# Kernel tuning notes

Hardware: AMD Instinct MI355X
Metric: run time of the kernel (lower is better)

## Reference

```python
import jax, jax.numpy as jnp
import numpy as np

N_HEADS = 16


def _rope(x, cos, sin):
    # x: (B,H,S,hd); cos,sin: (1,1,S,hd//2). Full-dim rotation (rot_dim == head_dim).
    xe = x[..., 0::2]
    xo = x[..., 1::2]
    re = xe * cos - xo * sin
    ro = xe * sin + xo * cos
    return jnp.stack([re, ro], axis=-1).reshape(x.shape)


def setup_inputs() -> dict:
    key = jax.random.key(0)
    B, S, D = 2, 2048, 1024
    hd = D // N_HEADS
    k1, k2, k3, k4, k5 = jax.random.split(key, 5)
    x = jax.random.normal(k1, (B, S, D), dtype=jnp.float32)
    # Linear params (lecun-normal-ish scale)
    w_qkv = jax.random.normal(k2, (D, 3 * D), dtype=jnp.float32) / np.sqrt(D)
    b_qkv = jnp.zeros((3 * D,), dtype=jnp.float32)
    w_out = jax.random.normal(k3, (D, D), dtype=jnp.float32) / np.sqrt(D)
    b_out = jnp.zeros((D,), dtype=jnp.float32)
    # Rotary tables: (S, hd//2)
    inv_freq = 1.0 / (10000.0 ** (np.arange(0, hd, 2, dtype=np.float32) / hd))
    angles = jnp.asarray(np.arange(S, dtype=np.float32)[:, None] * inv_freq[None, :])
    cos = jnp.cos(angles)
    sin = jnp.sin(angles)
    # Causal mask (seq, seq), True = attend
    mask = jnp.tril(jnp.ones((S, S), dtype=bool))
    return {"x": x, "w_qkv": w_qkv, "b_qkv": b_qkv, "w_out": w_out,
            "b_out": b_out, "cos": cos, "sin": sin, "mask": mask}


def reference(x, w_qkv, b_qkv, w_out, b_out, cos, sin, mask):
    B, S, D = x.shape
    H = N_HEADS
    hd = D // H
    scale = hd ** (-0.5)
    qkv = x @ w_qkv + b_qkv  # (B,S,3D)
    qkv = qkv.reshape(B, S, 3, H, hd).transpose(2, 0, 3, 1, 4)  # (3,B,H,S,hd)
    q, k, v = qkv[0], qkv[1], qkv[2]
    c = cos[None, None, :, :]
    s = sin[None, None, :, :]
    q = _rope(q, c, s)
    k = _rope(k, c, s)
    attn = jnp.einsum('bhqd,bhkd->bhqk', q, k) * scale
    attn = jnp.where(mask, attn, -1e9)
    attn = jax.nn.softmax(attn, axis=-1)
    out = jnp.einsum('bhqk,bhkd->bhqd', attn, v)
    out = out.transpose(0, 2, 1, 3).reshape(B, S, D)
    return out @ w_out + b_out
```

## Files before the change

### kernel.cpp

```cpp
#include <hip/hip_runtime.h>
#include <stdint.h>

typedef unsigned short u16;
typedef __attribute__((ext_vector_type(8))) __bf16 bf16x8;
typedef __attribute__((ext_vector_type(4))) float f32x4;
typedef __attribute__((ext_vector_type(4))) unsigned short u16x4;

__device__ __forceinline__ float bf2f(u16 u){
  unsigned int x = ((unsigned int)u) << 16;
  return __builtin_bit_cast(float, x);
}
__device__ __forceinline__ u16 f2bf(float f){
  return __builtin_bit_cast(u16, (__bf16)f);
}
__device__ __forceinline__ float fexp2(float x){ return __builtin_exp2f(x); }
__device__ __forceinline__ void lds_load16(const void* g, void* l){
  __builtin_amdgcn_global_load_lds(
      (const __attribute__((address_space(1))) unsigned int*)g,
      (__attribute__((address_space(3))) unsigned int*)l, 16, 0, 0);
}

__device__ __forceinline__ void transpose_body(const float* __restrict__ in,
                                               u16* __restrict__ out,
                                               int R, int C, int bx, int by,
                                               u16 (*t)[65]){
  const int c0 = bx * 64, r0 = by * 64;
  const int tid = threadIdx.x;
  const int rr = tid >> 3;
  const int cc = (tid & 7) * 8;
#pragma unroll
  for (int i = 0; i < 2; i++){
    int r = i * 32 + rr;
    const float* p = in + (size_t)(r0 + r) * C + c0 + cc;
    f32x4 v0 = *(const f32x4*)p;
    f32x4 v1 = *(const f32x4*)(p + 4);
#pragma unroll
    for (int j = 0; j < 4; j++){ t[r][cc + j] = f2bf(v0[j]); t[r][cc + 4 + j] = f2bf(v1[j]); }
  }
  __syncthreads();
#pragma unroll
  for (int i = 0; i < 2; i++){
    int c = i * 32 + rr;
    u16 tmp[8];
#pragma unroll
    for (int j = 0; j < 8; j++) tmp[j] = t[cc + j][c];
    *(bf16x8*)(out + (size_t)(c0 + c) * R + r0 + cc) = *(const bf16x8*)tmp;
  }
}

__global__ __launch_bounds__(256) void prep(const float* __restrict__ w_qkv,
                                            const float* __restrict__ w_out,
                                            const float* __restrict__ x,
                                            u16* __restrict__ wT1,
                                            u16* __restrict__ wT2,
                                            u16* __restrict__ xbf){
  __shared__ u16 t[64][65];
  const int bid = blockIdx.x;
  if (bid < 2048){
    int i = bid * 256 + threadIdx.x;
    const float* p = x + (size_t)i * 8;
    f32x4 v0 = *(const f32x4*)p;
    f32x4 v1 = *(const f32x4*)(p + 4);
    u16 tmp[8];
#pragma unroll
    for (int j = 0; j < 4; j++){ tmp[j] = f2bf(v0[j]); tmp[4 + j] = f2bf(v1[j]); }
    *(bf16x8*)(xbf + (size_t)i * 8) = *(const bf16x8*)tmp;
  } else if (bid < 2048 + 768){
    int idx = bid - 2048;
    transpose_body(w_qkv, wT1, 1024, 3072, idx % 48, idx / 48, t);
  } else {
    int idx = bid - 2816;
    transpose_body(w_out, wT2, 1024, 1024, idx % 16, idx / 16, t);
  }
}

__global__ __launch_bounds__(256) void v_transpose(const u16* __restrict__ qkv,
                                                   u16* __restrict__ vT){
  const int S = 2048, LD = 3072;
  __shared__ u16 t[64][65];
  const int bh = blockIdx.y;
  const int b = bh >> 4, h = bh & 15;
  const int s0 = blockIdx.x * 64;
  const u16* src = qkv + (size_t)b * S * LD + 2048 + h * 64;
  const int tid = threadIdx.x;
  const int rr = tid >> 3;
  const int cc = (tid & 7) * 8;
#pragma unroll
  for (int i = 0; i < 2; i++){
    int s = i * 32 + rr;
    bf16x8 v = *(const bf16x8*)(src + (size_t)(s0 + s) * LD + cc);
#pragma unroll
    for (int j = 0; j < 8; j++) t[s][cc + j] = __builtin_bit_cast(u16, (__bf16)v[j]);
  }
  __syncthreads();
  u16* dst = vT + (size_t)bh * 64 * S;
#pragma unroll
  for (int i = 0; i < 2; i++){
    int d = i * 32 + rr;
    u16 tmp[8];
#pragma unroll
    for (int j = 0; j < 8; j++) tmp[j] = t[cc + j][d];
    *(bf16x8*)(dst + (size_t)d * S + s0 + cc) = *(const bf16x8*)tmp;
  }
}

template<bool OUTF32, bool ROPE>
__global__ __launch_bounds__(256, 3) void gemm_bt(const u16* __restrict__ A,
                                                  const u16* __restrict__ Bt,
                                                  const float* __restrict__ bias,
                                                  void* __restrict__ Cv,
                                                  int M, int N, int K,
                                                  const float* __restrict__ cosb,
                                                  const float* __restrict__ sinb){
  __shared__ u16 As[128 * 32];
  __shared__ u16 Bs[128 * 32];
  const int nx = gridDim.x;
  const int L = blockIdx.x + nx * blockIdx.y;
  const int per = (nx * gridDim.y) >> 3;
  const int wg = (L & 7) * per + (L >> 3);
  const int bn = wg % nx, bm = wg / nx;
  const int tid = threadIdx.x, w = tid >> 6, l = tid & 63;
  const int lo = l & 15, hi = l >> 4;
  const int wr = (w >> 1) * 64, wc = (w & 1) * 64;
  f32x4 acc[4][4] = {};
  const int lrow = l >> 2, lcd = l & 3;

  for (int k0 = 0; k0 < K; k0 += 32){
#pragma unroll
    for (int i = 0; i < 2; i++){
      int row0 = i * 64 + w * 16;
      int row = row0 + lrow;
      int cs = lcd ^ ((row >> 1) & 3);
      lds_load16(A  + (size_t)(bm * 128 + row) * K + k0 + cs * 8,
                 (char*)As + row0 * 64);
      lds_load16(Bt + (size_t)(bn * 128 + row) * K + k0 + cs * 8,
                 (char*)Bs + row0 * 64);
    }
    __syncthreads();
    bf16x8 a[4], b[4];
#pragma unroll
    for (int mi = 0; mi < 4; mi++){
      int row = wr + mi * 16 + lo;
      unsigned byte = (unsigned)(row * 64 + hi * 16) ^ (((row >> 1) & 3) << 4);
      a[mi] = *(const bf16x8*)((const char*)As + byte);
    }
#pragma unroll
    for (int ni = 0; ni < 4; ni++){
      int row = wc + ni * 16 + lo;
      unsigned byte = (unsigned)(row * 64 + hi * 16) ^ (((row >> 1) & 3) << 4);
      b[ni] = *(const bf16x8*)((const char*)Bs + byte);
    }
    __builtin_amdgcn_s_setprio(1);
#pragma unroll
    for (int mi = 0; mi < 4; mi++)
#pragma unroll
      for (int ni = 0; ni < 4; ni++)
        acc[mi][ni] = __builtin_amdgcn_mfma_f32_16x16x32_bf16(a[mi], b[ni], acc[mi][ni], 0, 0, 0);
    __builtin_amdgcn_s_setprio(0);
    __syncthreads();
  }
  if (ROPE && bn < 16){
#pragma unroll
    for (int mi = 0; mi < 4; mi++){
#pragma unroll
      for (int r = 0; r < 4; r++){
        int grow = bm * 128 + wr + mi * 16 + hi * 4 + r;
        int stok = grow & 2047;
#pragma unroll
        for (int ni = 0; ni < 4; ni++){
          int col = bn * 128 + wc + ni * 16 + lo;
          float v = acc[mi][ni][r] + bias[col];
          float partner = __shfl_xor(v, 1, 64);
          int ip = (col & 63) >> 1;
          float c = cosb[stok * 32 + ip], sn = sinb[stok * 32 + ip];
          float res = (lo & 1) ? (partner * sn + v * c) : (v * c - partner * sn);
          ((u16*)Cv)[(size_t)grow * N + col] = f2bf(res);
        }
      }
    }
  } else {
#pragma unroll
    for (int mi = 0; mi < 4; mi++){
#pragma unroll
      for (int r = 0; r < 4; r++){
        int grow = bm * 128 + wr + mi * 16 + hi * 4 + r;
#pragma unroll
        for (int ni = 0; ni < 4; ni++){
          int col = bn * 128 + wc + ni * 16 + lo;
          float v = acc[mi][ni][r] + bias[col];
          if (OUTF32)
            ((float*)Cv)[(size_t)grow * N + col] = v;
          else
            ((u16*)Cv)[(size_t)grow * N + col] = f2bf(v);
        }
      }
    }
  }
}

#define FA_PHASE(T_, OA_, OB_, MA_, MB_, LA_, LB_)                             \
  {                                                                            \
    const int q0p = (T_) * 32;                                                 \
    const int qrA = q0p + lo, qrB = q0p + 16 + lo;                             \
    const int nkt = (T_) + 1;                                                  \
    const int ch = (nkt + 1) >> 1;                                             \
    const int k0 = w ? ch : 0;                                                 \
    const int k1 = w ? nkt : ch;                                               \
    bf16x8 qfA0, qfA1, qfB0, qfB1;                                             \
    {                                                                          \
      bf16x8 va0 = *(const bf16x8*)(Qp + (size_t)qrA * LD + hi * 8);           \
      bf16x8 va1 = *(const bf16x8*)(Qp + (size_t)qrA * LD + 32 + hi * 8);      \
      bf16x8 vb0 = *(const bf16x8*)(Qp + (size_t)qrB * LD + hi * 8);           \
      bf16x8 vb1 = *(const bf16x8*)(Qp + (size_t)qrB * LD + 32 + hi * 8);      \
      _Pragma("unroll")                                                        \
      for (int j = 0; j < 8; j++){                                             \
        qfA0[j] = (__bf16)((float)va0[j] * QSC);                               \
        qfA1[j] = (__bf16)((float)va1[j] * QSC);                               \
        qfB0[j] = (__bf16)((float)vb0[j] * QSC);                               \
        qfB1[j] = (__bf16)((float)vb1[j] * QSC);                               \
      }                                                                        \
    }                                                                          \
    float lparA = 0.f, lparB = 0.f;                                            \
    MA_ = -1e30f; MB_ = -1e30f;                                                \
    if (k0 < k1){                                                              \
      _Pragma("unroll")                                                        \
      for (int i = 0; i < 4; i++)                                              \
        lds_load16(Kp + (size_t)(k0 * 32 + i * 8 + srow8) * LD + scs * 8,      \
                   (char*)&Ks[w][0][0] + i * 1024);                            \
    }                                                                          \
    int cur = 0;                                                               \
    for (int kt = k0; kt < k1; kt++){                                          \
      bf16x8 vb[4];                                                            \
      _Pragma("unroll")                                                        \
      for (int fd = 0; fd < 4; fd++)                                           \
        vb[fd] = *(const bf16x8*)(Vb + (size_t)(fd * 16 + lo) * S +            \
                                  kt * 32 + hi * 8);                           \
      bf16x8 kb[2][2];                                                         \
      _Pragma("unroll")                                                        \
      for (int c = 0; c < 2; c++){                                             \
        _Pragma("unroll")                                                      \
        for (int f = 0; f < 2; f++){                                           \
          int srw = f * 16 + lo;                                               \
          unsigned byte = ((unsigned)(srw * 128 + c * 64 + hi * 16)) ^         \
                          ((lo & 7) << 4);                                     \
          kb[c][f] = *(const bf16x8*)((const char*)&Ks[w][cur][0] + byte);     \
        }                                                                      \
      }                                                                        \
      if (kt + 1 < k1){                                                        \
        _Pragma("unroll")                                                      \
        for (int i = 0; i < 4; i++)                                            \
          lds_load16(Kp + (size_t)((kt + 1) * 32 + i * 8 + srow8) * LD +       \
                         scs * 8,                                              \
                     (char*)&Ks[w][cur ^ 1][0] + i * 1024);                    \
      }                                                                        \
      f32x4 saA[2] = {}, saB[2] = {};                                          \
      __builtin_amdgcn_s_setprio(1);                                           \
      _Pragma("unroll")                                                        \
      for (int f = 0; f < 2; f++){                                             \
        saA[f] = __builtin_amdgcn_mfma_f32_16x16x32_bf16(kb[0][f], qfA0,       \
                                                         saA[f], 0, 0, 0);     \
        saB[f] = __builtin_amdgcn_mfma_f32_16x16x32_bf16(kb[0][f], qfB0,       \
                                                         saB[f], 0, 0, 0);     \
        saA[f] = __builtin_amdgcn_mfma_f32_16x16x32_bf16(kb[1][f], qfA1,       \
                                                         saA[f], 0, 0, 0);     \
        saB[f] = __builtin_amdgcn_mfma_f32_16x16x32_bf16(kb[1][f], qfB1,       \
                                                         saB[f], 0, 0, 0);     \
      }                                                                        \
      __builtin_amdgcn_s_setprio(0);                                           \
      if (kt == nkt - 1){                                                      \
        _Pragma("unroll")                                                      \
        for (int f = 0; f < 2; f++){                                           \
          int key0 = kt * 32 + f * 16 + hi * 4;                                \
          _Pragma("unroll")                                                    \
          for (int r = 0; r < 4; r++){                                         \
            if (key0 + r > qrA) saA[f][r] = -1e30f;                            \
            if (key0 + r > qrB) saB[f][r] = -1e30f;                            \
          }                                                                    \
        }                                                                      \
      }                                                                        \
      float pmA = fmaxf(                                                       \
          fmaxf(fmaxf(saA[0][0], saA[0][1]), fmaxf(saA[0][2], saA[0][3])),     \
          fmaxf(fmaxf(saA[1][0], saA[1][1]), fmaxf(saA[1][2], saA[1][3])));    \
      float pmB = fmaxf(                                                       \
          fmaxf(fmaxf(saB[0][0], saB[0][1]), fmaxf(saB[0][2], saB[0][3])),     \
          fmaxf(fmaxf(saB[1][0], saB[1][1]), fmaxf(saB[1][2], saB[1][3])));    \
      if (!__all(fmaxf(pmA - MA_, pmB - MB_) <= 11.5f)){                       \
        float rmA = fmaxf(pmA, __shfl_xor(pmA, 16, 64));                       \
        rmA = fmaxf(rmA, __shfl_xor(rmA, 32, 64));                             \
        float rmB = fmaxf(pmB, __shfl_xor(pmB, 16, 64));                       \
        rmB = fmaxf(rmB, __shfl_xor(rmB, 32, 64));                             \
        float mnA = fmaxf(MA_, rmA), mnB = fmaxf(MB_, rmB);                    \
        float cA = fexp2(MA_ - mnA), cB = fexp2(MB_ - mnB);                    \
        MA_ = mnA; MB_ = mnB;                                                  \
        lparA *= cA; lparB *= cB;                                              \
        float cqA[4], cqB[4];                                                  \
        _Pragma("unroll")                                                      \
        for (int r = 0; r < 4; r++){                                           \
          cqA[r] = __shfl(cA, hi * 4 + r, 64);                                 \
          cqB[r] = __shfl(cB, hi * 4 + r, 64);                                 \
        }                                                                      \
        _Pragma("unroll")                                                      \
        for (int fd = 0; fd < 4; fd++){                                        \
          _Pragma("unroll")                                                    \
          for (int r = 0; r < 4; r++){                                         \
            OA_[fd][r] *= cqA[r]; OB_[fd][r] *= cqB[r];                        \
          }                                                                    \
        }                                                                      \
      }                                                                        \
      float pvA[2][4], pvB[2][4];                                              \
      _Pragma("unroll")                                                        \
      for (int f = 0; f < 2; f++){                                             \
        _Pragma("unroll")                                                      \
        for (int r = 0; r < 4; r++){                                           \
          pvA[f][r] = fexp2(saA[f][r] - MA_);                                  \
          pvB[f][r] = fexp2(saB[f][r] - MB_);                                  \
        }                                                                      \
      }                                                                        \
      _Pragma("unroll")                                                        \
      for (int f = 0; f < 2; f++){                                             \
        u16x4 pkA, pkB;                                                        \
        _Pragma("unroll")                                                      \
        for (int r = 0; r < 4; r++){                                           \
          pkA[r] = f2bf(pvA[f][r]); pkB[r] = f2bf(pvB[f][r]);                  \
        }                                                                      \
        *(u16x4*)((char*)&Ps[w][0][0] + lo * 72 + f * 32 + hi * 8) = pkA;      \
        *(u16x4*)((char*)&Ps[w][1][0] + lo * 72 + f * 32 + hi * 8) = pkB;      \
      }                                                                        \
      lparA += ((pvA[0][0] + pvA[0][1]) + (pvA[0][2] + pvA[0][3]))             \
             + ((pvA[1][0] + pvA[1][1]) + (pvA[1][2] + pvA[1][3]));            \
      lparB += ((pvB[0][0] + pvB[0][1]) + (pvB[0][2] + pvB[0][3]))             \
             + ((pvB[1][0] + pvB[1][1]) + (pvB[1][2] + pvB[1][3]));            \
      bf16x8 paA = *(const bf16x8*)((const char*)&Ps[w][0][0] + lo * 72 +      \
                                    hi * 16);                                  \
      bf16x8 paB = *(const bf16x8*)((const char*)&Ps[w][1][0] + lo * 72 +      \
                                    hi * 16);                                  \
      __builtin_amdgcn_s_setprio(1);                                           \
      _Pragma("unroll")                                                        \
      for (int fd = 0; fd < 4; fd++){                                          \
        OA_[fd] = __builtin_amdgcn_mfma_f32_16x16x32_bf16(paA, vb[fd],         \
                                                          OA_[fd], 0, 0, 0);   \
        OB_[fd] = __builtin_amdgcn_mfma_f32_16x16x32_bf16(paB, vb[fd],         \
                                                          OB_[fd], 0, 0, 0);   \
      }                                                                        \
      __builtin_amdgcn_s_setprio(0);                                           \
      cur ^= 1;                                                                \
    }                                                                          \
    lparA += __shfl_xor(lparA, 16, 64); lparA += __shfl_xor(lparA, 32, 64);    \
    lparB += __shfl_xor(lparB, 16, 64); lparB += __shfl_xor(lparB, 32, 64);    \
    LA_ = lparA; LB_ = lparB;                                                  \
  }

#define FA_WRITEPART(slot_, OA_, OB_, MA_, MB_, LA_, LB_)                      \
  {                                                                            \
    _Pragma("unroll")                                                          \
    for (int fd = 0; fd < 4; fd++){                                            \
      u16x4 pkA, pkB;                                                          \
      _Pragma("unroll")                                                        \
      for (int r = 0; r < 4; r++){                                             \
        pkA[r] = f2bf(OA_[fd][r]); pkB[r] = f2bf(OB_[fd][r]);                  \
      }                                                                        \
      *(u16x4*)((char*)&Xo[slot_][0] + (fd * 16 + lo) * 72 + hi * 8) = pkA;    \
      *(u16x4*)((char*)&Xo[slot_][0] + (fd * 16 + lo) * 72 + 32 + hi * 8) = pkB;\
    }                                                                          \
    if (hi == 0){                                                              \
      Xm[slot_][lo] = MA_;      Xl[slot_][lo] = LA_;                           \
      Xm[slot_][16 + lo] = MB_; Xl[slot_][16 + lo] = LB_;                      \
    }                                                                          \
  }

#define FA_COMBINE(slot_, T_, OA_, OB_, MA_, MB_, LA_, LB_)                    \
  {                                                                            \
    const int q0p = (T_) * 32;                                                 \
    u16x4 pA[4], pB[4];                                                        \
    _Pragma("unroll")                                                          \
    for (int fd = 0; fd < 4; fd++){                                            \
      pA[fd] = *(const u16x4*)((const char*)&Xo[slot_][0] +                    \
                               (fd * 16 + lo) * 72 + hi * 8);                  \
      pB[fd] = *(const u16x4*)((const char*)&Xo[slot_][0] +                    \
                               (fd * 16 + lo) * 72 + 32 + hi * 8);             \
    }                                                                          \
    _Pragma("unroll")                                                          \
    for (int r = 0; r < 4; r++){                                               \
      float mOA = __shfl(MA_, hi * 4 + r, 64);                                 \
      float lOA = __shfl(LA_, hi * 4 + r, 64);                                 \
      float mOB = __shfl(MB_, hi * 4 + r, 64);                                 \
      float lOB = __shfl(LB_, hi * 4 + r, 64);                                 \
      float mPA = Xm[slot_][hi * 4 + r], lPA = Xl[slot_][hi * 4 + r];          \
      float mPB = Xm[slot_][16 + hi * 4 + r], lPB = Xl[slot_][16 + hi * 4 + r];\
      float MfA = fmaxf(mOA, mPA), MfB = fmaxf(mOB, mPB);                      \
      float c0A = fexp2(mOA - MfA), c1A = fexp2(mPA - MfA);                    \
      float c0B = fexp2(mOB - MfB), c1B = fexp2(mPB - MfB);                    \
      float invA = 1.0f / (lOA * c0A + lPA * c1A);                             \
      float invB = 1.0f / (lOB * c0B + lPB * c1B);                             \
      int srA = q0p + hi * 4 + r;                                              \
      int srB = q0p + 16 + hi * 4 + r;                                         \
      u16* orA = Oout + (size_t)(b * S + srA) * 1024 + h * 64;                 \
      u16* orB = Oout + (size_t)(b * S + srB) * 1024 + h * 64;                 \
      _Pragma("unroll")                                                        \
      for (int fd = 0; fd < 4; fd++){                                          \
        float vA = (OA_[fd][r] * c0A + bf2f(pA[fd][r]) * c1A) * invA;          \
        float vB = (OB_[fd][r] * c0B + bf2f(pB[fd][r]) * c1B) * invB;          \
        orA[fd * 16 + lo] = f2bf(vA);                                          \
        orB[fd * 16 + lo] = f2bf(vB);                                          \
      }                                                                        \
    }                                                                          \
  }

__global__ __launch_bounds__(128, 2) void flash_attn(const u16* __restrict__ qkv,
                                                     const u16* __restrict__ vT,
                                                     u16* __restrict__ Oout){
  const int S = 2048, LD = 3072;
  const int L = blockIdx.x;
  const int bh = L & 31;
  const int bx = L >> 5;
  const int b = bh >> 4, h = bh & 15;
  const u16* base = qkv + (size_t)b * S * LD;
  const u16* Qp = base + h * 64;
  const u16* Kp = base + 1024 + h * 64;
  const u16* Vb = vT + (size_t)bh * 64 * S;
  const int tid = threadIdx.x, w = tid >> 6, l = tid & 63;
  const int lo = l & 15, hi = l >> 4;
  __shared__ u16 Ks[2][2][32 * 64];
  __shared__ u16 Ps[2][2][16 * 36];
  __shared__ u16 Xo[2][64 * 36];
  __shared__ float Xm[2][32], Xl[2][32];

  const float QSC = 0.125f * 1.44269504089f;
  const int srow8 = l >> 3;
  const int scs = (l & 7) ^ srow8;

  f32x4 o1A[4] = {}, o1B[4] = {};
  f32x4 o2A[4] = {}, o2B[4] = {};
  float m1A, m1B, l1A, l1B, m2A, m2B, l2A, l2B;

  FA_PHASE(63 - bx, o1A, o1B, m1A, m1B, l1A, l1B);
  if (w == 1) FA_WRITEPART(0, o1A, o1B, m1A, m1B, l1A, l1B);
  FA_PHASE(bx,      o2A, o2B, m2A, m2B, l2A, l2B);
  if (w == 0) FA_WRITEPART(1, o2A, o2B, m2A, m2B, l2A, l2B);
  __syncthreads();
  if (w == 0){
    FA_COMBINE(0, 63 - bx, o1A, o1B, m1A, m1B, l1A, l1B);
  } else {
    FA_COMBINE(1, bx,      o2A, o2B, m2A, m2B, l2A, l2B);
  }
}

extern "C" void kernel_launch(void* const* d_in, const int* in_sizes, int n_in,
                              void* d_out, int out_size, void* d_ws, size_t ws_size,
                              hipStream_t stream){
  const float* x     = (const float*)d_in[0];
  const float* w_qkv = (const float*)d_in[1];
  const float* b_qkv = (const float*)d_in[2];
  const float* w_out = (const float*)d_in[3];
  const float* b_out = (const float*)d_in[4];
  const float* cosb  = (const float*)d_in[5];
  const float* sinb  = (const float*)d_in[6];
  float* out = (float*)d_out;
  char* ws = (char*)d_ws;
  u16* qkv  = (u16*)(ws);
  u16* attn = (u16*)(ws + 25165824);
  u16* xbf  = attn;
  u16* wT2  = (u16*)(ws + 33554432);
  u16* wT1  = (u16*)(ws + 35651584);
  u16* vT   = (u16*)(ws + 35651584);

  prep<<<3072, 256, 0, stream>>>(w_qkv, w_out, x, wT1, wT2, xbf);
  gemm_bt<false, true ><<<dim3(24, 32), 256, 0, stream>>>(xbf, wT1, b_qkv, qkv,
                                                          4096, 3072, 1024, cosb, sinb);
  v_transpose<<<dim3(32, 32), 256, 0, stream>>>(qkv, vT);
  flash_attn<<<1024, 128, 0, stream>>>(qkv, vT, attn);
  gemm_bt<true , false><<<dim3(8, 32), 256, 0, stream>>>(attn, wT2, b_out, out,
                                                         4096, 1024, 1024, cosb, sinb);
}
```

Measured before the change: 129.3 us.

## Deepen K prefetch pipeline with register double-buffered LDS reads in flash attention

Restructures the attention K loop into a manually unrolled two-iteration body. The next tile's K fragments are read from LDS into alternate register sets during the current QK MFMAs, and the global-to-LDS staging is issued two tiles ahead. This aims to hide LDS read latency and global load latency behind MFMA work. It adds register pressure and relies on the LDS double buffer being consistent, since no explicit waits are visible between staging and reading.

```diff
diff --git a/kernel.cpp b/kernel.cpp
--- a/kernel.cpp
+++ b/kernel.cpp
@@ -198,6 +198,123 @@
   }
 }
 
+#define FA_DSREAD(KB_, KT_)                                                    \
+  { _Pragma("unroll")                                                          \
+    for (int c = 0; c < 2; c++){                                               \
+      _Pragma("unroll")                                                        \
+      for (int f = 0; f < 2; f++){                                             \
+        int srw = f * 16 + lo;                                                 \
+        unsigned byte = ((unsigned)(srw * 128 + c * 64 + hi * 16)) ^           \
+                        ((lo & 7) << 4);                                       \
+        KB_[c * 2 + f] = *(const bf16x8*)(                                     \
+            (const char*)&Ks[w][(KT_) & 1][0] + byte);                         \
+      } } }
+
+#define FA_STAGE(KT_)                                                          \
+  { _Pragma("unroll")                                                          \
+    for (int i = 0; i < 4; i++)                                                \
+      lds_load16(Kp + (size_t)((KT_) * 32 + i * 8 + srow8) * LD + scs * 8,     \
+                 (char*)&Ks[w][(KT_) & 1][0] + i * 1024); }
+
+#define FA_BODY(KBU_, KBL_, KT_, OA_, OB_, MA_, MB_)                           \
+  {                                                                            \
+    bf16x8 vb[4];                                                              \
+    _Pragma("unroll")                                                          \
+    for (int fd = 0; fd < 4; fd++)                                             \
+      vb[fd] = *(const bf16x8*)(Vb + (size_t)(fd * 16 + lo) * S +              \
+                                (KT_) * 32 + hi * 8);                          \
+    if ((KT_) + 1 < k1) FA_DSREAD(KBL_, (KT_) + 1);                            \
+    f32x4 saA[2] = {}, saB[2] = {};                                            \
+    __builtin_amdgcn_s_setprio(1);                                             \
+    saA[0] = __builtin_amdgcn_mfma_f32_16x16x32_bf16(KBU_[0], qfA0, saA[0], 0, 0, 0); \
+    saB[0] = __builtin_amdgcn_mfma_f32_16x16x32_bf16(KBU_[0], qfB0, saB[0], 0, 0, 0); \
+    saA[0] = __builtin_amdgcn_mfma_f32_16x16x32_bf16(KBU_[2], qfA1, saA[0], 0, 0, 0); \
+    saB[0] = __builtin_amdgcn_mfma_f32_16x16x32_bf16(KBU_[2], qfB1, saB[0], 0, 0, 0); \
+    saA[1] = __builtin_amdgcn_mfma_f32_16x16x32_bf16(KBU_[1], qfA0, saA[1], 0, 0, 0); \
+    saB[1] = __builtin_amdgcn_mfma_f32_16x16x32_bf16(KBU_[1], qfB0, saB[1], 0, 0, 0); \
+    saA[1] = __builtin_amdgcn_mfma_f32_16x16x32_bf16(KBU_[3], qfA1, saA[1], 0, 0, 0); \
+    saB[1] = __builtin_amdgcn_mfma_f32_16x16x32_bf16(KBU_[3], qfB1, saB[1], 0, 0, 0); \
+    __builtin_amdgcn_s_setprio(0);                                             \
+    __builtin_amdgcn_sched_barrier(0);                                         \
+    if ((KT_) + 2 < k1) FA_STAGE((KT_) + 2);                                   \
+    if ((KT_) == nkt - 1){                                                     \
+      _Pragma("unroll")                                                        \
+      for (int f = 0; f < 2; f++){                                             \
+        int key0 = (KT_) * 32 + f * 16 + hi * 4;                               \
+        _Pragma("unroll")                                                      \
+        for (int r = 0; r < 4; r++){                                           \
+          if (key0 + r > qrA) saA[f][r] = -1e30f;                              \
+          if (key0 + r > qrB) saB[f][r] = -1e30f;                              \
+        }                                                                      \
+      }                                                                        \
+    }                                                                          \
+    float pmA = fmaxf(                                                         \
+        fmaxf(fmaxf(saA[0][0], saA[0][1]), fmaxf(saA[0][2], saA[0][3])),       \
+        fmaxf(fmaxf(saA[1][0], saA[1][1]), fmaxf(saA[1][2], saA[1][3])));      \
+    float pmB = fmaxf(                                                         \
+        fmaxf(fmaxf(saB[0][0], saB[0][1]), fmaxf(saB[0][2], saB[0][3])),       \
+        fmaxf(fmaxf(saB[1][0], saB[1][1]), fmaxf(saB[1][2], saB[1][3])));      \
+    if (!__all(fmaxf(pmA - MA_, pmB - MB_) <= 11.5f)){                         \
+      float rmA = fmaxf(pmA, __shfl_xor(pmA, 16, 64));                         \
+      rmA = fmaxf(rmA, __shfl_xor(rmA, 32, 64));                               \
+      float rmB = fmaxf(pmB, __shfl_xor(pmB, 16, 64));                         \
+      rmB = fmaxf(rmB, __shfl_xor(rmB, 32, 64));                               \
+      float mnA = fmaxf(MA_, rmA), mnB = fmaxf(MB_, rmB);                      \
+      float cA = fexp2(MA_ - mnA), cB = fexp2(MB_ - mnB);                      \
+      MA_ = mnA; MB_ = mnB;                                                    \
+      lparA *= cA; lparB *= cB;                                                \
+      float cqA[4], cqB[4];                                                    \
+      _Pragma("unroll")                                                        \
+      for (int r = 0; r < 4; r++){                                             \
+        cqA[r] = __shfl(cA, hi * 4 + r, 64);                                   \
+        cqB[r] = __shfl(cB, hi * 4 + r, 64);                                   \
+      }                                                                        \
+      _Pragma("unroll")                                                        \
+      for (int fd = 0; fd < 4; fd++){                                          \
+        _Pragma("unroll")                                                      \
+        for (int r = 0; r < 4; r++){                                           \
+          OA_[fd][r] *= cqA[r]; OB_[fd][r] *= cqB[r];                          \
+        }                                                                      \
+      }                                                                        \
+    }                                                                          \
+    float pvA[2][4], pvB[2][4];                                                \
+    _Pragma("unroll")                                                          \
+    for (int f = 0; f < 2; f++){                                               \
+      _Pragma("unroll")                                                        \
+      for (int r = 0; r < 4; r++){                                             \
+        pvA[f][r] = fexp2(saA[f][r] - MA_);                                    \
+        pvB[f][r] = fexp2(saB[f][r] - MB_);                                    \
+      }                                                                        \
+    }                                                                          \
+    _Pragma("unroll")                                                          \
+    for (int f = 0; f < 2; f++){                                               \
+      u16x4 pkA, pkB;                                                          \
+      _Pragma("unroll")                                                        \
+      for (int r = 0; r < 4; r++){                                             \
+        pkA[r] = f2bf(pvA[f][r]); pkB[r] = f2bf(pvB[f][r]);                    \
+      }                                                                        \
+      *(u16x4*)((char*)&Ps[w][0][0] + lo * 72 + f * 32 + hi * 8) = pkA;        \
+      *(u16x4*)((char*)&Ps[w][1][0] + lo * 72 + f * 32 + hi * 8) = pkB;        \
+    }                                                                          \
+    lparA += ((pvA[0][0] + pvA[0][1]) + (pvA[0][2] + pvA[0][3]))               \
+           + ((pvA[1][0] + pvA[1][1]) + (pvA[1][2] + pvA[1][3]));              \
+    lparB += ((pvB[0][0] + pvB[0][1]) + (pvB[0][2] + pvB[0][3]))               \
+           + ((pvB[1][0] + pvB[1][1]) + (pvB[1][2] + pvB[1][3]));              \
+    bf16x8 paA = *(const bf16x8*)((const char*)&Ps[w][0][0] + lo * 72 +        \
+                                  hi * 16);                                    \
+    bf16x8 paB = *(const bf16x8*)((const char*)&Ps[w][1][0] + lo * 72 +        \
+                                  hi * 16);                                    \
+    __builtin_amdgcn_s_setprio(1);                                             \
+    _Pragma("unroll")                                                          \
+    for (int fd = 0; fd < 4; fd++){                                            \
+      OA_[fd] = __builtin_amdgcn_mfma_f32_16x16x32_bf16(paA, vb[fd],           \
+                                                        OA_[fd], 0, 0, 0);     \
+      OB_[fd] = __builtin_amdgcn_mfma_f32_16x16x32_bf16(paB, vb[fd],           \
+                                                        OB_[fd], 0, 0, 0);     \
+    }                                                                          \
+    __builtin_amdgcn_s_setprio(0);                                             \
+  }
+
 #define FA_PHASE(T_, OA_, OB_, MA_, MB_, LA_, LB_)                             \
   {                                                                            \
     const int q0p = (T_) * 32;                                                 \
@@ -222,128 +339,20 @@
     }                                                                          \
     float lparA = 0.f, lparB = 0.f;                                            \
     MA_ = -1e30f; MB_ = -1e30f;                                                \
-    if (k0 < k1){                                                              \
-      _Pragma("unroll")                                                        \
-      for (int i = 0; i < 4; i++)                                              \
-        lds_load16(Kp + (size_t)(k0 * 32 + i * 8 + srow8) * LD + scs * 8,      \
-                   (char*)&Ks[w][0][0] + i * 1024);                            \
-    }                                                                          \
-    int cur = 0;                                                               \
-    for (int kt = k0; kt < k1; kt++){                                          \
-      bf16x8 vb[4];                                                            \
-      _Pragma("unroll")                                                        \
-      for (int fd = 0; fd < 4; fd++)                                           \
-        vb[fd] = *(const bf16x8*)(Vb + (size_t)(fd * 16 + lo) * S +            \
-                                  kt * 32 + hi * 8);                           \
-      bf16x8 kb[2][2];                                                         \
-      _Pragma("unroll")                                                        \
-      for (int c = 0; c < 2; c++){                                             \
-        _Pragma("unroll")                                                      \
-        for (int f = 0; f < 2; f++){                                           \
-          int srw = f * 16 + lo;                                               \
-          unsigned byte = ((unsigned)(srw * 128 + c * 64 + hi * 16)) ^         \
-                          ((lo & 7) << 4);                                     \
-          kb[c][f] = *(const bf16x8*)((const char*)&Ks[w][cur][0] + byte);     \
-        }                                                                      \
-      }                                                                        \
-      if (kt + 1 < k1){                                                        \
-        _Pragma("unroll")                                                      \
-        for (int i = 0; i < 4; i++)                                            \
-          lds_load16(Kp + (size_t)((kt + 1) * 32 + i * 8 + srow8) * LD +       \
-                         scs * 8,                                              \
-                     (char*)&Ks[w][cur ^ 1][0] + i * 1024);                    \
-      }                                                                        \
-      f32x4 saA[2] = {}, saB[2] = {};                                          \
-      __builtin_amdgcn_s_setprio(1);                                           \
-      _Pragma("unroll")                                                        \
-      for (int f = 0; f < 2; f++){                                             \
-        saA[f] = __builtin_amdgcn_mfma_f32_16x16x32_bf16(kb[0][f], qfA0,       \
-                                                         saA[f], 0, 0, 0);     \
-        saB[f] = __builtin_amdgcn_mfma_f32_16x16x32_bf16(kb[0][f], qfB0,       \
-                                                         saB[f], 0, 0, 0);     \
-        saA[f] = __builtin_amdgcn_mfma_f32_16x16x32_bf16(kb[1][f], qfA1,       \
-                                                         saA[f], 0, 0, 0);     \
-        saB[f] = __builtin_amdgcn_mfma_f32_16x16x32_bf16(kb[1][f], qfB1,       \
-                                                         saB[f], 0, 0, 0);     \
-      }                                                                        \
-      __builtin_amdgcn_s_setprio(0);                                           \
-      if (kt == nkt - 1){                                                      \
-        _Pragma("unroll")                                                      \
-        for (int f = 0; f < 2; f++){                                           \
-          int key0 = kt * 32 + f * 16 + hi * 4;                                \
-          _Pragma("unroll")                                                    \
-          for (int r = 0; r < 4; r++){                                         \
-            if (key0 + r > qrA) saA[f][r] = -1e30f;                            \
-            if (key0 + r > qrB) saB[f][r] = -1e30f;                            \
-          }                                                                    \
-        }                                                                      \
-      }                                                                        \
-      float pmA = fmaxf(                                                       \
-          fmaxf(fmaxf(saA[0][0], saA[0][1]), fmaxf(saA[0][2], saA[0][3])),     \
-          fmaxf(fmaxf(saA[1][0], saA[1][1]), fmaxf(saA[1][2], saA[1][3])));    \
-      float pmB = fmaxf(                                                       \
-          fmaxf(fmaxf(saB[0][0], saB[0][1]), fmaxf(saB[0][2], saB[0][3])),     \
-          fmaxf(fmaxf(saB[1][0], saB[1][1]), fmaxf(saB[1][2], saB[1][3])));    \
-      if (!__all(fmaxf(pmA - MA_, pmB - MB_) <= 11.5f)){                       \
-        float rmA = fmaxf(pmA, __shfl_xor(pmA, 16, 64));                       \
-        rmA = fmaxf(rmA, __shfl_xor(rmA, 32, 64));                             \
-        float rmB = fmaxf(pmB, __shfl_xor(pmB, 16, 64));                       \
-        rmB = fmaxf(rmB, __shfl_xor(rmB, 32, 64));                             \
-        float mnA = fmaxf(MA_, rmA), mnB = fmaxf(MB_, rmB);                    \
-        float cA = fexp2(MA_ - mnA), cB = fexp2(MB_ - mnB);                    \
-        MA_ = mnA; MB_ = mnB;                                                  \
-        lparA *= cA; lparB *= cB;                                              \
-        float cqA[4], cqB[4];                                                  \
-        _Pragma("unroll")                                                      \
-        for (int r = 0; r < 4; r++){                                           \
-          cqA[r] = __shfl(cA, hi * 4 + r, 64);                                 \
-          cqB[r] = __shfl(cB, hi * 4 + r, 64);                                 \
-        }                                                                      \
-        _Pragma("unroll")                                                      \
-        for (int fd = 0; fd < 4; fd++){                                        \
-          _Pragma("unroll")                                                    \
-          for (int r = 0; r < 4; r++){                                         \
-            OA_[fd][r] *= cqA[r]; OB_[fd][r] *= cqB[r];                        \
-          }                                                                    \
-        }                                                                      \
-      }                                                                        \
-      float pvA[2][4], pvB[2][4];                                              \
-      _Pragma("unroll")                                                        \
-      for (int f = 0; f < 2; f++){                                             \
-        _Pragma("unroll")                                                      \
-        for (int r = 0; r < 4; r++){                                           \
-          pvA[f][r] = fexp2(saA[f][r] - MA_);                                  \
-          pvB[f][r] = fexp2(saB[f][r] - MB_);                                  \
-        }                                                                      \
-      }                                                                        \
-      _Pragma("unroll")                                                        \
-      for (int f = 0; f < 2; f++){                                             \
-        u16x4 pkA, pkB;                                                        \
-        _Pragma("unroll")                                                      \
-        for (int r = 0; r < 4; r++){                                           \
-          pkA[r] = f2bf(pvA[f][r]); pkB[r] = f2bf(pvB[f][r]);                  \
-        }                                                                      \
-        *(u16x4*)((char*)&Ps[w][0][0] + lo * 72 + f * 32 + hi * 8) = pkA;      \
-        *(u16x4*)((char*)&Ps[w][1][0] + lo * 72 + f * 32 + hi * 8) = pkB;      \
-      }                                                                        \
-      lparA += ((pvA[0][0] + pvA[0][1]) + (pvA[0][2] + pvA[0][3]))             \
-             + ((pvA[1][0] + pvA[1][1]) + (pvA[1][2] + pvA[1][3]));            \
-      lparB += ((pvB[0][0] + pvB[0][1]) + (pvB[0][2] + pvB[0][3]))             \
-             + ((pvB[1][0] + pvB[1][1]) + (pvB[1][2] + pvB[1][3]));            \
-      bf16x8 paA = *(const bf16x8*)((const char*)&Ps[w][0][0] + lo * 72 +      \
-                                    hi * 16);                                  \
-      bf16x8 paB = *(const bf16x8*)((const char*)&Ps[w][1][0] + lo * 72 +      \
-                                    hi * 16);                                  \
-      __builtin_amdgcn_s_setprio(1);                                           \
-      _Pragma("unroll")                                                        \
-      for (int fd = 0; fd < 4; fd++){                                          \
-        OA_[fd] = __builtin_amdgcn_mfma_f32_16x16x32_bf16(paA, vb[fd],         \
-                                                          OA_[fd], 0, 0, 0);   \
-        OB_[fd] = __builtin_amdgcn_mfma_f32_16x16x32_bf16(paB, vb[fd],         \
-                                                          OB_[fd], 0, 0, 0);   \
-      }                                                                        \
-      __builtin_amdgcn_s_setprio(0);                                           \
-      cur ^= 1;                                                                \
+    bf16x8 kbA[4], kbB[4];                                                     \
+    int kt = k0;                                                               \
+    if (kt < k1){                                                              \
+      FA_STAGE(kt);                                                            \
+      if (kt + 1 < k1) FA_STAGE(kt + 1);                                       \
+      FA_DSREAD(kbA, kt);                                                      \
+      while (true){                                                            \
+        FA_BODY(kbA, kbB, kt, OA_, OB_, MA_, MB_);                             \
+        kt++;                                                                  \
+        if (kt >= k1) break;                                                   \
+        FA_BODY(kbB, kbA, kt, OA_, OB_, MA_, MB_);                             \
+        kt++;                                                                  \
+        if (kt >= k1) break;                                                   \
+      }                                                                        \
     }                                                                          \
     lparA += __shfl_xor(lparA, 16, 64); lparA += __shfl_xor(lparA, 32, 64);    \
     lparB += __shfl_xor(lparB, 16, 64); lparB += __shfl_xor(lparB, 32, 64);    \
```

After: 124.3 us, median of 2. 1.04x faster.
